# Kernel tuning notes

Hardware: AMD Instinct MI355X
Metric: run time of the kernel (lower is better)

## Reference

```python
import jax, jax.numpy as jnp
import numpy as np

LOG2 = 16          # log2_num_embeddings
VQ_DIM = 32        # vq_dim
EMB_DIM = 512      # embedding_dim
TEMPERATURE = 1.0
EPS = 1e-8


def setup_inputs() -> dict:
    key = jax.random.key(0)
    k = jax.random.split(key, 7)
    h = jax.random.normal(k[0], (32, 2048, EMB_DIM), dtype=jnp.float32)
    attn_mask = jax.random.randint(k[1], (32, 2048), 0, 2).astype(jnp.int32)
    # proj: Linear(EMB_DIM, VQ_DIM); stored as [in, out]
    W_proj = jax.random.normal(k[2], (EMB_DIM, VQ_DIM), dtype=jnp.float32) * 0.02
    b_proj = jnp.zeros((VQ_DIM,), dtype=jnp.float32)
    # proj_inv: Linear(VQ_DIM, EMB_DIM); stored as [in, out]
    W_inv = jax.random.normal(k[3], (VQ_DIM, EMB_DIM), dtype=jnp.float32) * 0.02
    b_inv = jnp.zeros((EMB_DIM,), dtype=jnp.float32)
    # codebook: 2*LOG2 rows of VQ_DIM
    emb = jax.random.normal(k[4], (2 * LOG2, VQ_DIM), dtype=jnp.float32)
    return {"h": h, "attn_mask": attn_mask, "W_proj": W_proj, "b_proj": b_proj,
            "W_inv": W_inv, "b_inv": b_inv, "emb": emb}


def reference(h, attn_mask, W_proj, b_proj, W_inv, b_inv, emb):
    B, L, _ = h.shape
    M = 2 * LOG2
    # project + L2-normalize (with eps, as in forward)
    hp = jnp.einsum('ble,ed->bld', h, W_proj) + b_proj
    hn = hp / (jnp.linalg.norm(hp, axis=-1, keepdims=True) + EPS)
    # normalize codebook rows (with eps, as in forward)
    E = emb / (jnp.linalg.norm(emb, axis=-1, keepdims=True) + EPS)
    # pairwise squared distances [B, L, M]
    d = (jnp.sum(hn * hn, axis=-1, keepdims=True)
         + jnp.sum(E * E, axis=-1)
         - 2.0 * jnp.einsum('bld,md->blm', hn, E))
    # group-wise (pairs of 2) softmax
    dp = d.reshape(B, L, LOG2, 2)
    A = jax.nn.softmax(-dp / TEMPERATURE, axis=-1)            # [B, L, LOG2, 2]
    code = jnp.argmax(A, axis=-1)                              # [B, L, LOG2] int
    # train mode: soft assignment h_vq = A @ E
    h_vq = jnp.einsum('blm,md->bld', A.reshape(B, L, M), E)    # [B, L, VQ_DIM]
    mask = (attn_mask == 1)
    quantized = jnp.where(mask[..., None], h_vq, 0.0)
    quantized = jnp.einsum('bld,de->ble', quantized, W_inv) + b_inv
    # binary code -> integer id, zeroed at masked-out positions
    shift = 2 ** jnp.arange(LOG2, dtype=jnp.int64)
    vq_code = jnp.where(mask, jnp.sum(code.astype(jnp.int64) * shift, axis=-1), 0)
    vq_loss = jnp.float32(0.0)
    return quantized, vq_code, vq_loss
```

## Files before the change

### kernel.cpp

```cpp
#include <hip/hip_runtime.h>
#include <math.h>

#define EMB 512
#define VQ 32
#define MCODES 32
#define EPS 1e-8f

#define KSTEP 32
#define NSTEPS 16
#define TILE 128
#define HSTRIDE 1040
#define HBUFSZ (16 * HSTRIDE)
#define WBUFSZ 4096
#define HOFF0 0
#define HOFF1 HBUFSZ
#define WOFF0 (2 * HBUFSZ)
#define WOFF1 (2 * HBUFSZ + WBUFSZ)
#define LDS_TOTAL (2 * HBUFSZ + 2 * WBUFSZ)

#define ACC4(A, V)                                                        \
    A.x += V.x * w0.x; A.x += V.y * w1.x; A.x += V.z * w2.x; A.x += V.w * w3.x; \
    A.y += V.x * w0.y; A.y += V.y * w1.y; A.y += V.z * w2.y; A.y += V.w * w3.y; \
    A.z += V.x * w0.z; A.z += V.y * w1.z; A.z += V.z * w2.z; A.z += V.w * w3.z; \
    A.w += V.x * w0.w; A.w += V.y * w1.w; A.w += V.z * w2.w; A.w += V.w * w3.w;

__global__ __launch_bounds__(256)
void prep_kernel(const float* __restrict__ emb, const float* __restrict__ W_inv,
                 float* __restrict__ Cw, float* __restrict__ G, float* __restrict__ qv,
                 float* __restrict__ loss_out) {
  const int b = blockIdx.x;
  const int tid = threadIdx.x;
  __shared__ float En_s[VQ];
  float ss = 0.f;
#pragma unroll
  for (int d = 0; d < VQ; ++d) { float v = emb[b * VQ + d]; ss += v * v; }
  const float inv = 1.0f / (sqrtf(ss) + EPS);
  if (tid < VQ) En_s[tid] = emb[b * VQ + tid] * inv;
  __syncthreads();
  float a0 = 0.f, a1 = 0.f;
#pragma unroll 8
  for (int d = 0; d < VQ; ++d) {
    const float en = En_s[d];
    const float2 wv = ((const float2*)(W_inv + d * EMB))[tid];
    a0 += en * wv.x;
    a1 += en * wv.y;
  }
  ((float2*)(Cw + b * EMB))[tid] = make_float2(a0, a1);
  if (tid < VQ) G[b * VQ + tid] = 2.0f * En_s[tid];
  if (tid == 0) {
    float qq = 0.f;
#pragma unroll
    for (int d = 0; d < VQ; ++d) qq += En_s[d] * En_s[d];
    qv[b] = qq;
    if (b == 0) loss_out[0] = 0.0f;
  }
}

__global__ __launch_bounds__(256)
void proj_kernel(const float* __restrict__ h, const int* __restrict__ mask,
                 const float* __restrict__ W_proj, const float* __restrict__ b_proj,
                 const float* __restrict__ G, const float* __restrict__ qv,
                 float* __restrict__ Aout, float* __restrict__ code_out) {
  const int tid = threadIdx.x;
  const int w = tid >> 6;
  const int lane = tid & 63;
  const int dg = tid & 7;
  const int ts = tid >> 3;
  const int tile = blockIdx.x * TILE;

  __shared__ __align__(16) char lds[LDS_TOTAL];

  const int hoff[2] = {HOFF0, HOFF1};
  const int woff[2] = {WOFF0, WOFF1};

  const int srow = lane >> 3;
  const int scol = (lane & 7) * 4;

  auto stage = [&](int b, int s) {
#pragma unroll
    for (int i = 0; i < 4; ++i) {
      const int c = 4 * w + i;
      const float* g = h + (size_t)(tile + 8 * c + srow) * EMB + s * KSTEP + scol;
      char* l = &lds[hoff[b] + c * HSTRIDE];
      __builtin_amdgcn_global_load_lds((const __attribute__((address_space(1))) void*)g,
                                       (__attribute__((address_space(3))) void*)l, 16, 0, 0);
    }
    {
      const float* g = W_proj + (size_t)(s * KSTEP + 8 * w + srow) * VQ + scol;
      char* l = &lds[woff[b] + w * 1024];
      __builtin_amdgcn_global_load_lds((const __attribute__((address_space(1))) void*)g,
                                       (__attribute__((address_space(3))) void*)l, 16, 0, 0);
    }
  };

  float4 a0 = make_float4(0.f, 0.f, 0.f, 0.f), a1 = a0, a2 = a0, a3 = a0;
  const int hrowbase = (ts >> 1) * HSTRIDE + (ts & 1) * 512;

  stage(0, 0);
  __syncthreads();

  int b = 0;
  for (int s = 0; s < NSTEPS; ++s) {
    if (s + 1 < NSTEPS) stage(b ^ 1, s + 1);
    const char* hb = &lds[hoff[b]];
    const char* wb = &lds[woff[b]];
#pragma unroll
    for (int kf = 0; kf < 8; ++kf) {
      const float4 w0 = *(const float4*)(wb + (4 * kf + 0) * 128 + dg * 16);
      const float4 w1 = *(const float4*)(wb + (4 * kf + 1) * 128 + dg * 16);
      const float4 w2 = *(const float4*)(wb + (4 * kf + 2) * 128 + dg * 16);
      const float4 w3 = *(const float4*)(wb + (4 * kf + 3) * 128 + dg * 16);
      const float4 v0 = *(const float4*)(hb + hrowbase + 0 * 128 + kf * 16);
      const float4 v1 = *(const float4*)(hb + hrowbase + 1 * 128 + kf * 16);
      const float4 v2 = *(const float4*)(hb + hrowbase + 2 * 128 + kf * 16);
      const float4 v3 = *(const float4*)(hb + hrowbase + 3 * 128 + kf * 16);
      ACC4(a0, v0) ACC4(a1, v1) ACC4(a2, v2) ACC4(a3, v3)
    }
    __syncthreads();
    b ^= 1;
  }

  float* part = (float*)lds;
  *(float4*)&part[(4 * ts + 0) * 36 + dg * 4] = a0;
  *(float4*)&part[(4 * ts + 1) * 36 + dg * 4] = a1;
  *(float4*)&part[(4 * ts + 2) * 36 + dg * 4] = a2;
  *(float4*)&part[(4 * ts + 3) * 36 + dg * 4] = a3;
  __syncthreads();

  if (tid < 128) {
    const int t = tile + tid;
    const float4* bp4 = (const float4*)b_proj;
    float4 hp[8];
    float ssum = 0.f;
#pragma unroll
    for (int k = 0; k < 8; ++k) {
      float4 v = *(const float4*)&part[tid * 36 + k * 4];
      const float4 bb = bp4[k];
      v.x += bb.x; v.y += bb.y; v.z += bb.z; v.w += bb.w;
      hp[k] = v;
      ssum += v.x * v.x + v.y * v.y + v.z * v.z + v.w * v.w;
    }
    const float inv = 1.0f / (sqrtf(ssum) + EPS);
#pragma unroll
    for (int k = 0; k < 8; ++k) {
      hp[k].x *= inv; hp[k].y *= inv; hp[k].z *= inv; hp[k].w *= inv;
    }
    const float4* G4 = (const float4*)G;
    float av[32];
    int code = 0;
#pragma unroll
    for (int g = 0; g < 16; ++g) {
      float d0 = 0.f, d1 = 0.f;
#pragma unroll
      for (int k = 0; k < 8; ++k) {
        const float4 g0 = G4[(2 * g) * 8 + k];
        const float4 g1 = G4[(2 * g + 1) * 8 + k];
        const float4 hv = hp[k];
        d0 += hv.x * g0.x + hv.y * g0.y + hv.z * g0.z + hv.w * g0.w;
        d1 += hv.x * g1.x + hv.y * g1.y + hv.z * g1.z + hv.w * g1.w;
      }
      const float s0 = d0 - qv[2 * g];
      const float s1 = d1 - qv[2 * g + 1];
      const float mx = fmaxf(s0, s1);
      const float e0 = expf(s0 - mx);
      const float e1 = expf(s1 - mx);
      const float rs = 1.0f / (e0 + e1);
      av[2 * g] = e0 * rs;
      av[2 * g + 1] = e1 * rs;
      code |= (e1 > e0) ? (1 << g) : 0;
    }
    const int mk = mask[t];
    const float msk = (mk == 1) ? 1.0f : 0.0f;
    float4* Ao = (float4*)(Aout + (size_t)t * MCODES);
#pragma unroll
    for (int k = 0; k < 8; ++k) {
      Ao[k] = make_float4(av[4 * k] * msk, av[4 * k + 1] * msk,
                          av[4 * k + 2] * msk, av[4 * k + 3] * msk);
    }
    code_out[t] = (mk == 1) ? (float)code : 0.0f;
  }
}

__global__ __launch_bounds__(256)
void inv_kernel(const float* __restrict__ Ap, const float* __restrict__ Cw,
                const float* __restrict__ b_inv, float* __restrict__ qout) {
  const int tid = threadIdx.x;
  const int w = tid >> 6;
  const int lane = tid & 63;
  const int ep = w * 64 + lane;
  const int tile = blockIdx.x * 64;
  float2 c[32];
#pragma unroll
  for (int m = 0; m < 32; ++m) c[m] = ((const float2*)(Cw + m * EMB))[ep];
  const float2 bi = ((const float2*)b_inv)[ep];
  for (int tt = 0; tt < 64; ++tt) {
    const int t = tile + tt;
    const float4* a4 = (const float4*)(Ap + (size_t)t * 32);
    float accx = bi.x, accy = bi.y;
#pragma unroll
    for (int k = 0; k < 8; ++k) {
      const float4 a = a4[k];
      accx += a.x * c[4 * k].x + a.y * c[4 * k + 1].x + a.z * c[4 * k + 2].x + a.w * c[4 * k + 3].x;
      accy += a.x * c[4 * k].y + a.y * c[4 * k + 1].y + a.z * c[4 * k + 2].y + a.w * c[4 * k + 3].y;
    }
    ((float2*)(qout + (size_t)t * EMB))[ep] = make_float2(accx, accy);
  }
}

extern "C" void kernel_launch(void* const* d_in, const int* in_sizes, int n_in,
                              void* d_out, int out_size, void* d_ws, size_t ws_size,
                              hipStream_t stream) {
  (void)n_in; (void)out_size; (void)ws_size;
  const float* h      = (const float*)d_in[0];
  const int*   mask   = (const int*)  d_in[1];
  const float* W_proj = (const float*)d_in[2];
  const float* b_proj = (const float*)d_in[3];
  const float* W_inv  = (const float*)d_in[4];
  const float* b_inv  = (const float*)d_in[5];
  const float* emb    = (const float*)d_in[6];

  const int N = in_sizes[1];

  float* quant    = (float*)d_out;
  float* code_out = quant + (size_t)N * EMB;
  float* loss_out = code_out + N;

  float* ws = (float*)d_ws;
  float* Ap = ws;
  float* Cw = Ap + (size_t)N * MCODES;
  float* G  = Cw + MCODES * EMB;
  float* qv = G + MCODES * VQ;

  prep_kernel<<<MCODES, 256, 0, stream>>>(emb, W_inv, Cw, G, qv, loss_out);
  proj_kernel<<<N / TILE, 256, 0, stream>>>(h, mask, W_proj, b_proj, G, qv, Ap, code_out);
  inv_kernel<<<N / 64, 256, 0, stream>>>(Ap, Cw, b_inv, quant);
}
```

Baseline: 104.5 us.

## Triple-buffer projection staging with vmcnt waits and one barrier per step

Changes the LDS staging in the projection kernel from double to triple buffering, keeping two K-steps of async global-to-LDS loads in flight. Each step now waits with an explicit s_waitcnt vmcnt(5) for only the oldest stage, then uses a single s_barrier, replacing the two __syncthreads per step. The aim is to hide global load latency for h and to cut barrier overhead. In exchange, LDS per block grows by about half, which may lower the number of resident blocks per CU, and correctness depends on the hand-counted vmcnt matching the five loads issued per stage.

```diff
diff --git a/kernel.cpp b/kernel.cpp
--- a/kernel.cpp
+++ b/kernel.cpp
@@ -12,11 +12,7 @@
 #define HSTRIDE 1040
 #define HBUFSZ (16 * HSTRIDE)
 #define WBUFSZ 4096
-#define HOFF0 0
-#define HOFF1 HBUFSZ
-#define WOFF0 (2 * HBUFSZ)
-#define WOFF1 (2 * HBUFSZ + WBUFSZ)
-#define LDS_TOTAL (2 * HBUFSZ + 2 * WBUFSZ)
+#define LDS_TOTAL (3 * HBUFSZ + 3 * WBUFSZ)
 
 #define ACC4(A, V)                                                        \
     A.x += V.x * w0.x; A.x += V.y * w1.x; A.x += V.z * w2.x; A.x += V.w * w3.x; \
@@ -70,24 +66,23 @@
 
   __shared__ __align__(16) char lds[LDS_TOTAL];
 
-  const int hoff[2] = {HOFF0, HOFF1};
-  const int woff[2] = {WOFF0, WOFF1};
-
   const int srow = lane >> 3;
   const int scol = (lane & 7) * 4;
 
-  auto stage = [&](int b, int s) {
+  auto stage = [&](int bi, int s) {
+    const int hbase = bi * HBUFSZ;
+    const int wbase = 3 * HBUFSZ + bi * WBUFSZ;
 #pragma unroll
     for (int i = 0; i < 4; ++i) {
       const int c = 4 * w + i;
       const float* g = h + (size_t)(tile + 8 * c + srow) * EMB + s * KSTEP + scol;
-      char* l = &lds[hoff[b] + c * HSTRIDE];
+      char* l = &lds[hbase + c * HSTRIDE];
       __builtin_amdgcn_global_load_lds((const __attribute__((address_space(1))) void*)g,
                                        (__attribute__((address_space(3))) void*)l, 16, 0, 0);
     }
     {
       const float* g = W_proj + (size_t)(s * KSTEP + 8 * w + srow) * VQ + scol;
-      char* l = &lds[woff[b] + w * 1024];
+      char* l = &lds[wbase + w * 1024];
       __builtin_amdgcn_global_load_lds((const __attribute__((address_space(1))) void*)g,
                                        (__attribute__((address_space(3))) void*)l, 16, 0, 0);
     }
@@ -97,13 +92,21 @@
   const int hrowbase = (ts >> 1) * HSTRIDE + (ts & 1) * 512;
 
   stage(0, 0);
-  __syncthreads();
-
-  int b = 0;
+  stage(1, 1);
+
+  int cur = 0;
   for (int s = 0; s < NSTEPS; ++s) {
-    if (s + 1 < NSTEPS) stage(b ^ 1, s + 1);
-    const char* hb = &lds[hoff[b]];
-    const char* wb = &lds[woff[b]];
+    if (s < NSTEPS - 1) { asm volatile("s_waitcnt vmcnt(5)" ::: "memory"); }
+    else               { asm volatile("s_waitcnt vmcnt(0)" ::: "memory"); }
+    __builtin_amdgcn_sched_barrier(0);
+    __builtin_amdgcn_s_barrier();
+    __builtin_amdgcn_sched_barrier(0);
+    if (s + 2 < NSTEPS) {
+      const int nxt2 = (cur >= 1) ? cur - 1 : 2;
+      stage(nxt2, s + 2);
+    }
+    const char* hb = &lds[cur * HBUFSZ];
+    const char* wb = &lds[3 * HBUFSZ + cur * WBUFSZ];
 #pragma unroll
     for (int kf = 0; kf < 8; ++kf) {
       const float4 w0 = *(const float4*)(wb + (4 * kf + 0) * 128 + dg * 16);
@@ -116,9 +119,9 @@
       const float4 v3 = *(const float4*)(hb + hrowbase + 3 * 128 + kf * 16);
       ACC4(a0, v0) ACC4(a1, v1) ACC4(a2, v2) ACC4(a3, v3)
     }
-    __syncthreads();
-    b ^= 1;
-  }
+    cur = (cur < 2) ? cur + 1 : 0;
+  }
+  __syncthreads();
 
   float* part = (float*)lds;
   *(float4*)&part[(4 * ts + 0) * 36 + dg * 4] = a0;
```

New measurement: 106.7 us. 1.02x slower.
